# Kernel tuning notes

Hardware: AMD Instinct MI355X
Metric: run time of the kernel (lower is better)

The kernel has to match this reference:

```python
import jax, jax.numpy as jnp
import numpy as np

C = 256
C8 = C // 8

def setup_inputs() -> dict:
    key = jax.random.key(0)
    ks = jax.random.split(key, 8)
    B, H, W = 4, 64, 64
    x = jax.random.normal(ks[0], (B, C, H, W), dtype=jnp.float32)
    wq = jax.random.normal(ks[1], (C8, C), dtype=jnp.float32) * (1.0 / np.sqrt(C))
    bq = jnp.zeros((C8,), dtype=jnp.float32)
    wk = jax.random.normal(ks[2], (C8, C), dtype=jnp.float32) * (1.0 / np.sqrt(C))
    bk = jnp.zeros((C8,), dtype=jnp.float32)
    wv = jax.random.normal(ks[3], (C, C), dtype=jnp.float32) * (1.0 / np.sqrt(C))
    bv = jnp.zeros((C,), dtype=jnp.float32)
    gamma = jnp.ones((1,), dtype=jnp.float32) * 0.5  # nonzero so attention path contributes
    return {"x": x, "wq": wq, "bq": bq, "wk": wk, "bk": bk, "wv": wv, "bv": bv, "gamma": gamma}

def reference(x, wq, bq, wk, bk, wv, bv, gamma):
    B, Cc, Hh, Ww = x.shape
    N = Hh * Ww
    xf = x.reshape(B, Cc, N)  # [B,C,N]
    # 1x1 convs == per-pixel linear maps
    q = jnp.einsum('oc,bcn->bon', wq, xf) + bq[None, :, None]  # [B,C8,N]
    k = jnp.einsum('oc,bcn->bon', wk, xf) + bk[None, :, None]  # [B,C8,N]
    v = jnp.einsum('oc,bcn->bon', wv, xf) + bv[None, :, None]  # [B,C,N]
    # energy[b,n,m] = sum_c q[b,c,n] * k[b,c,m]  (unscaled)
    energy = jnp.einsum('bcn,bcm->bnm', q, k)
    attn = jax.nn.softmax(energy, axis=-1)
    # out[b,c,n] = sum_m v[b,c,m] * attn[b,n,m]
    out = jnp.einsum('bcm,bnm->bcn', v, attn).reshape(B, Cc, Hh, Ww)
    return gamma * out + x
```

## Files before the change

### kernel.cpp

```cpp
#include <hip/hip_runtime.h>
#include <hip/hip_fp16.h>

#define CC   256
#define QKC  32
#define NPIX 4096
#define NB   4
#define XSTR 264
#define VSTR 72

typedef __attribute__((ext_vector_type(8))) _Float16 f16x8;
typedef __attribute__((ext_vector_type(4))) float     f32x4;

__global__ __launch_bounds__(256) void wh_prep(
    const float* __restrict__ wq, const float* __restrict__ wk,
    const float* __restrict__ wv, __half* __restrict__ Wh)
{
    const int idx4 = blockIdx.x * 256 + threadIdx.x;
    const int o  = idx4 >> 6;
    const int cw = (idx4 & 63) << 2;
    const float* src;
    if (o < 256)      src = wv + (size_t)o * 256 + cw;
    else if (o < 288) src = wq + (size_t)(o - 256) * 256 + cw;
    else              src = wk + (size_t)(o - 288) * 256 + cw;
    const float4 v = *reinterpret_cast<const float4*>(src);
    __half h[4] = {__float2half(v.x), __float2half(v.y),
                   __float2half(v.z), __float2half(v.w)};
    *reinterpret_cast<uint2*>(Wh + (size_t)o * 256 + cw) =
        *reinterpret_cast<const uint2*>(h);
}

__global__ __launch_bounds__(512) void qkv_mfma(
    const float* __restrict__ x, const __half* __restrict__ Wh,
    const float* __restrict__ bq, const float* __restrict__ bk,
    const float* __restrict__ bv,
    __half* __restrict__ Qh, __half* __restrict__ Kh, __half* __restrict__ VTh)
{
    __shared__ __align__(16) __half sm[CC * VSTR];
    __half* xT   = sm;
    __half* vres = sm;

    const int t  = threadIdx.x;
    const int b  = blockIdx.x >> 6;
    const int n0 = (blockIdx.x & 63) << 6;

    {
        const int nl4 = t & 15;
        const int c0  = t >> 4;
        const float* xp = x + ((size_t)b * CC) * NPIX + n0 + nl4 * 4;
        #pragma unroll
        for (int i = 0; i < 8; ++i) {
            const int c = c0 + 32 * i;
            const float4 v = *reinterpret_cast<const float4*>(xp + (size_t)c * NPIX);
            xT[(nl4 * 4 + 0) * XSTR + c] = __float2half(v.x);
            xT[(nl4 * 4 + 1) * XSTR + c] = __float2half(v.y);
            xT[(nl4 * 4 + 2) * XSTR + c] = __float2half(v.z);
            xT[(nl4 * 4 + 3) * XSTR + c] = __float2half(v.w);
        }
    }
    __syncthreads();

    const int w = t >> 6, l = t & 63, lr = l & 15, s = l >> 4;
    const int nto = (w < 4) ? 3 : 2;
    const int ob0 = 32 * w, ob1 = 32 * w + 16, ob2 = 256 + 16 * w;

    f16x8 wf[3][8];
    #pragma unroll
    for (int kk = 0; kk < 8; ++kk) {
        wf[0][kk] = *reinterpret_cast<const f16x8*>(
            Wh + (size_t)(ob0 + lr) * 256 + kk * 32 + s * 8);
        wf[1][kk] = *reinterpret_cast<const f16x8*>(
            Wh + (size_t)(ob1 + lr) * 256 + kk * 32 + s * 8);
    }
    if (w < 4)
        #pragma unroll
        for (int kk = 0; kk < 8; ++kk)
            wf[2][kk] = *reinterpret_cast<const f16x8*>(
                Wh + (size_t)(ob2 + lr) * 256 + kk * 32 + s * 8);

    f32x4 acc[3][4];
    #pragma unroll
    for (int j = 0; j < 3; ++j)
        #pragma unroll
        for (int nt = 0; nt < 4; ++nt) acc[j][nt] = (f32x4){0.f, 0.f, 0.f, 0.f};

    #pragma unroll
    for (int nt = 0; nt < 4; ++nt) {
        f16x8 xf[8];
        #pragma unroll
        for (int kk = 0; kk < 8; ++kk)
            xf[kk] = *reinterpret_cast<const f16x8*>(
                &xT[(nt * 16 + lr) * XSTR + kk * 32 + s * 8]);
        #pragma unroll
        for (int j = 0; j < 3; ++j)
            if (j < nto)
                #pragma unroll
                for (int kk = 0; kk < 8; ++kk)
                    acc[j][nt] = __builtin_amdgcn_mfma_f32_16x16x32_f16(
                        xf[kk], wf[j][kk], acc[j][nt], 0, 0, 0);
    }

    if (w < 4) {
        const bool is_q = (w < 2);
        const int oc = (w & 1) * 16 + lr;
        __half* dst = is_q ? Qh : Kh;
        const float bias = (is_q ? bq : bk)[oc];
        #pragma unroll
        for (int nt = 0; nt < 4; ++nt)
            #pragma unroll
            for (int r = 0; r < 4; ++r) {
                const size_t n = (size_t)b * NPIX + n0 + nt * 16 + s * 4 + r;
                dst[n * QKC + oc] = __float2half(acc[2][nt][r] + bias);
            }
    }

    __syncthreads();
    {
        #pragma unroll
        for (int j = 0; j < 2; ++j) {
            const int c = 32 * w + 16 * j + lr;
            const float bias = bv[c];
            #pragma unroll
            for (int nt = 0; nt < 4; ++nt) {
                __half h[4];
                #pragma unroll
                for (int r = 0; r < 4; ++r) h[r] = __float2half(acc[j][nt][r] + bias);
                *reinterpret_cast<uint2*>(&vres[c * VSTR + nt * 16 + s * 4]) =
                    *reinterpret_cast<const uint2*>(h);
            }
        }
    }
    __syncthreads();
    {
        const int c = t >> 1, half = t & 1;
        __half* dst = VTh + ((size_t)(b * CC + c)) * NPIX + n0 + half * 32;
        #pragma unroll
        for (int jj = 0; jj < 4; ++jj)
            *reinterpret_cast<uint4*>(dst + jj * 8) =
                *reinterpret_cast<const uint4*>(&vres[c * VSTR + half * 32 + jj * 8]);
    }
}

__global__ __launch_bounds__(512) void attn_mfma(
    const __half* __restrict__ Qh, const __half* __restrict__ Kh,
    const __half* __restrict__ VTh, const float* __restrict__ x,
    const float* __restrict__ gamma, float* __restrict__ out)
{
    __shared__ unsigned char Praw[2][64 * 128];
    __shared__ float abuf[2][64];
    __shared__ float lbuf[64];

    const int t  = threadIdx.x;
    const int w  = t >> 6;
    const int l  = t & 63;
    const int lr = l & 15;
    const int s  = l >> 4;

    const int blk = (blockIdx.x & 7) * 32 + (blockIdx.x >> 3);
    const int b  = blk >> 6;
    const int n0 = (blk & 63) << 6;

    const int qw = w * 16 + lr;
    f16x8 qfrag;
    f16x8 kf[4];
    float m_run = -1e30f, l_run = 0.f;
    const __half* kbase = Kh + ((size_t)b * NPIX + lr) * QKC + s * 8;

    const int cbase = 64 * (w - 4);
    const __half* vbase = VTh + ((size_t)(b * CC + cbase + lr)) * NPIX + s * 8;
    f16x8 vfc[4][2], vfn[4][2];
    f32x4 O[4][4];
    #pragma unroll
    for (int ct = 0; ct < 4; ++ct)
        #pragma unroll
        for (int qt = 0; qt < 4; ++qt)
            O[ct][qt] = (f32x4){0.f, 0.f, 0.f, 0.f};

    auto do_softmax = [&](int bw) {
        f32x4 sacc[4];
        #pragma unroll
        for (int mt = 0; mt < 4; ++mt)
            sacc[mt] = __builtin_amdgcn_mfma_f32_16x16x32_f16(
                kf[mt], qfrag, (f32x4){0.f, 0.f, 0.f, 0.f}, 0, 0, 0);
        float tmax = sacc[0][0];
        #pragma unroll
        for (int mt = 0; mt < 4; ++mt)
            #pragma unroll
            for (int r = 0; r < 4; ++r) tmax = fmaxf(tmax, sacc[mt][r]);
        tmax = fmaxf(tmax, __shfl_xor(tmax, 16));
        tmax = fmaxf(tmax, __shfl_xor(tmax, 32));
        const float mnew = fmaxf(m_run, tmax);
        const float al   = __expf(m_run - mnew);
        float p[4][4];
        float lsum = 0.f;
        #pragma unroll
        for (int mt = 0; mt < 4; ++mt)
            #pragma unroll
            for (int r = 0; r < 4; ++r) {
                p[mt][r] = __expf(sacc[mt][r] - mnew);
                lsum += p[mt][r];
            }
        lsum += __shfl_xor(lsum, 16);
        lsum += __shfl_xor(lsum, 32);
        l_run = al * l_run + lsum;
        m_run = mnew;
        unsigned char* pb = &Praw[bw][0];
        #pragma unroll
        for (int mt = 0; mt < 4; ++mt) {
            const int g = ((s >> 1) + 2 * mt) ^ (qw & 7);
            const __half2 u0 = __floats2half2_rn(p[mt][0], p[mt][1]);
            const __half2 u1 = __floats2half2_rn(p[mt][2], p[mt][3]);
            *reinterpret_cast<__half2*>(pb + qw * 128 + g * 16 + (s & 1) * 8)     = u0;
            *reinterpret_cast<__half2*>(pb + qw * 128 + g * 16 + (s & 1) * 8 + 4) = u1;
        }
        if (l < 16) abuf[bw][qw] = al;
    };

    if (w < 4) {
        qfrag = *reinterpret_cast<const f16x8*>(
            Qh + ((size_t)b * NPIX + n0 + qw) * QKC + s * 8);
        #pragma unroll
        for (int mt = 0; mt < 4; ++mt)
            kf[mt] = *reinterpret_cast<const f16x8*>(kbase + (size_t)(mt * 16) * QKC);
        do_softmax(0);
        #pragma unroll
        for (int mt = 0; mt < 4; ++mt)
            kf[mt] = *reinterpret_cast<const f16x8*>(kbase + (size_t)(64 + mt * 16) * QKC);
    } else {
        #pragma unroll
        for (int ct = 0; ct < 4; ++ct)
            #pragma unroll
            for (int ks = 0; ks < 2; ++ks)
                vfc[ct][ks] = *reinterpret_cast<const f16x8*>(
                    vbase + (size_t)ct * 16 * NPIX + ks * 32);
    }
    __syncthreads();

    for (int step = 0; step < 64; ++step) {
        const int pbuf = step & 1;
        if (w < 4) {
            if (step < 63) {
                do_softmax(pbuf ^ 1);
                if (step < 62) {
                    const size_t moff = (size_t)((step + 2) * 64) * QKC;
                    #pragma unroll
                    for (int mt = 0; mt < 4; ++mt)
                        kf[mt] = *reinterpret_cast<const f16x8*>(
                            kbase + moff + (size_t)(mt * 16) * QKC);
                }
            }
        } else {
            if (step < 63) {
                const size_t moff = (size_t)((step + 1) * 64);
                #pragma unroll
                for (int ct = 0; ct < 4; ++ct)
                    #pragma unroll
                    for (int ks = 0; ks < 2; ++ks)
                        vfn[ct][ks] = *reinterpret_cast<const f16x8*>(
                            vbase + (size_t)ct * 16 * NPIX + moff + ks * 32);
            }
            float av[4];
            #pragma unroll
            for (int qt = 0; qt < 4; ++qt) av[qt] = abuf[pbuf][qt * 16 + lr];
            #pragma unroll
            for (int ct = 0; ct < 4; ++ct)
                #pragma unroll
                for (int qt = 0; qt < 4; ++qt)
                    #pragma unroll
                    for (int r = 0; r < 4; ++r) O[ct][qt][r] *= av[qt];

            const unsigned char* pr = &Praw[pbuf][0];
            #pragma unroll
            for (int qt = 0; qt < 4; ++qt) {
                const int q2 = qt * 16 + lr;
                const int g0 = s ^ (q2 & 7);
                const int g1 = (s + 4) ^ (q2 & 7);
                const f16x8 pf0 = *reinterpret_cast<const f16x8*>(pr + q2 * 128 + g0 * 16);
                const f16x8 pf1 = *reinterpret_cast<const f16x8*>(pr + q2 * 128 + g1 * 16);
                #pragma unroll
                for (int ct = 0; ct < 4; ++ct) {
                    O[ct][qt] = __builtin_amdgcn_mfma_f32_16x16x32_f16(
                        vfc[ct][0], pf0, O[ct][qt], 0, 0, 0);
                    O[ct][qt] = __builtin_amdgcn_mfma_f32_16x16x32_f16(
                        vfc[ct][1], pf1, O[ct][qt], 0, 0, 0);
                }
            }
            if (step < 63) {
                #pragma unroll
                for (int ct = 0; ct < 4; ++ct)
                    #pragma unroll
                    for (int ks = 0; ks < 2; ++ks) vfc[ct][ks] = vfn[ct][ks];
            }
        }
        __syncthreads();
    }

    if (w < 4) { if (l < 16) lbuf[qw] = l_run; }
    __syncthreads();
    if (w >= 4) {
        const float g = gamma[0];
        float linv[4];
        #pragma unroll
        for (int qt = 0; qt < 4; ++qt) linv[qt] = g / lbuf[qt * 16 + lr];
        #pragma unroll
        for (int ct = 0; ct < 4; ++ct)
            #pragma unroll
            for (int qt = 0; qt < 4; ++qt)
                #pragma unroll
                for (int r = 0; r < 4; ++r) {
                    const int c = cbase + ct * 16 + s * 4 + r;
                    const size_t idx = ((size_t)(b * CC + c)) * NPIX + n0 + qt * 16 + lr;
                    out[idx] = O[ct][qt][r] * linv[qt] + x[idx];
                }
    }
}

extern "C" void kernel_launch(void* const* d_in, const int* in_sizes, int n_in,
                              void* d_out, int out_size, void* d_ws, size_t ws_size,
                              hipStream_t stream) {
    const float* x     = (const float*)d_in[0];
    const float* wq    = (const float*)d_in[1];
    const float* bq    = (const float*)d_in[2];
    const float* wk    = (const float*)d_in[3];
    const float* bk    = (const float*)d_in[4];
    const float* wv    = (const float*)d_in[5];
    const float* bv    = (const float*)d_in[6];
    const float* gamma = (const float*)d_in[7];
    float* out = (float*)d_out;

    __half* Wh  = (__half*)d_ws;
    __half* Qh  = Wh + (size_t)320 * 256;
    __half* Kh  = Qh + (size_t)NB * NPIX * QKC;
    __half* VTh = Kh + (size_t)NB * NPIX * QKC;

    hipLaunchKernelGGL(wh_prep, dim3(80), dim3(256), 0, stream, wq, wk, wv, Wh);
    hipLaunchKernelGGL(qkv_mfma, dim3(NB * 64), dim3(512), 0, stream,
                       x, Wh, bq, bk, bv, Qh, Kh, VTh);
    hipLaunchKernelGGL(attn_mfma, dim3(256), dim3(512), 0, stream,
                       Qh, Kh, VTh, x, gamma, out);
}
```

Baseline: 101.0 us.

## Use exp2 softmax with lazy rescaling and ping-pong V registers

Folds log2(e) into the Q weights and bias so the softmax can use the native exp2 instruction. The online softmax now computes each lane's local max and exponentials before any cross-lane reduction, and skips rescaling the O accumulator unless the running max grows by more than a threshold, which a per-wave flag in shared memory signals. The step loop is unrolled by two with ping-pong V register buffers, which removes the register copy at each step, and MFMA priority is raised during the PV product. The trade-off is extra exp2 and shuffle work per tile and fp16 P values that can reach up to 2^8 before normalisation, which risks precision.

```diff
diff --git a/kernel.cpp b/kernel.cpp
--- a/kernel.cpp
+++ b/kernel.cpp
@@ -7,9 +7,16 @@
 #define NB   4
 #define XSTR 264
 #define VSTR 72
+#define LOG2E 1.44269504088896340736f
+#define TAU  8.0f
 
 typedef __attribute__((ext_vector_type(8))) _Float16 f16x8;
 typedef __attribute__((ext_vector_type(4))) float     f32x4;
+
+static __device__ __forceinline__ unsigned h2bits(__half2 h) {
+    union { __half2 h; unsigned u; } cv; cv.h = h; return cv.u;
+}
+#define E2(x) __builtin_amdgcn_exp2f(x)
 
 __global__ __launch_bounds__(256) void wh_prep(
     const float* __restrict__ wq, const float* __restrict__ wk,
@@ -19,12 +26,13 @@
     const int o  = idx4 >> 6;
     const int cw = (idx4 & 63) << 2;
     const float* src;
+    float scale = 1.0f;
     if (o < 256)      src = wv + (size_t)o * 256 + cw;
-    else if (o < 288) src = wq + (size_t)(o - 256) * 256 + cw;
+    else if (o < 288) { src = wq + (size_t)(o - 256) * 256 + cw; scale = LOG2E; }
     else              src = wk + (size_t)(o - 288) * 256 + cw;
     const float4 v = *reinterpret_cast<const float4*>(src);
-    __half h[4] = {__float2half(v.x), __float2half(v.y),
-                   __float2half(v.z), __float2half(v.w)};
+    __half h[4] = {__float2half(v.x * scale), __float2half(v.y * scale),
+                   __float2half(v.z * scale), __float2half(v.w * scale)};
     *reinterpret_cast<uint2*>(Wh + (size_t)o * 256 + cw) =
         *reinterpret_cast<const uint2*>(h);
 }
@@ -103,7 +111,7 @@
         const bool is_q = (w < 2);
         const int oc = (w & 1) * 16 + lr;
         __half* dst = is_q ? Qh : Kh;
-        const float bias = (is_q ? bq : bk)[oc];
+        const float bias = is_q ? bq[oc] * LOG2E : bk[oc];
         #pragma unroll
         for (int nt = 0; nt < 4; ++nt)
             #pragma unroll
@@ -147,6 +155,7 @@
 {
     __shared__ unsigned char Praw[2][64 * 128];
     __shared__ float abuf[2][64];
+    __shared__ __align__(16) int fbuf[2][4];
     __shared__ float lbuf[64];
 
     const int t  = threadIdx.x;
@@ -167,7 +176,7 @@
 
     const int cbase = 64 * (w - 4);
     const __half* vbase = VTh + ((size_t)(b * CC + cbase + lr)) * NPIX + s * 8;
-    f16x8 vfc[4][2], vfn[4][2];
+    f16x8 vA[4][2], vB[4][2];
     f32x4 O[4][4];
     #pragma unroll
     for (int ct = 0; ct < 4; ++ct)
@@ -181,38 +190,103 @@
         for (int mt = 0; mt < 4; ++mt)
             sacc[mt] = __builtin_amdgcn_mfma_f32_16x16x32_f16(
                 kf[mt], qfrag, (f32x4){0.f, 0.f, 0.f, 0.f}, 0, 0, 0);
-        float tmax = sacc[0][0];
+        float v[16];
         #pragma unroll
         for (int mt = 0; mt < 4; ++mt)
             #pragma unroll
-            for (int r = 0; r < 4; ++r) tmax = fmaxf(tmax, sacc[mt][r]);
-        tmax = fmaxf(tmax, __shfl_xor(tmax, 16));
-        tmax = fmaxf(tmax, __shfl_xor(tmax, 32));
-        const float mnew = fmaxf(m_run, tmax);
-        const float al   = __expf(m_run - mnew);
-        float p[4][4];
-        float lsum = 0.f;
-        #pragma unroll
-        for (int mt = 0; mt < 4; ++mt)
-            #pragma unroll
-            for (int r = 0; r < 4; ++r) {
-                p[mt][r] = __expf(sacc[mt][r] - mnew);
-                lsum += p[mt][r];
-            }
-        lsum += __shfl_xor(lsum, 16);
-        lsum += __shfl_xor(lsum, 32);
-        l_run = al * l_run + lsum;
-        m_run = mnew;
+            for (int r = 0; r < 4; ++r) v[mt * 4 + r] = sacc[mt][r];
+        float t8[8], t4[4], t2[2];
+        #pragma unroll
+        for (int i = 0; i < 8; ++i) t8[i] = fmaxf(v[i], v[i + 8]);
+        #pragma unroll
+        for (int i = 0; i < 4; ++i) t4[i] = fmaxf(t8[i], t8[i + 4]);
+        t2[0] = fmaxf(t4[0], t4[2]); t2[1] = fmaxf(t4[1], t4[3]);
+        const float m_l = fmaxf(t2[0], t2[1]);
+        float p[16];
+        #pragma unroll
+        for (int i = 0; i < 16; ++i) p[i] = E2(v[i] - m_l);
+        float s8[8], s4[4], s2[2];
+        #pragma unroll
+        for (int i = 0; i < 8; ++i) s8[i] = p[i] + p[i + 8];
+        #pragma unroll
+        for (int i = 0; i < 4; ++i) s4[i] = s8[i] + s8[i + 4];
+        s2[0] = s4[0] + s4[2]; s2[1] = s4[1] + s4[3];
+        const float e_l = s2[0] + s2[1];
+        float m_p = __shfl_xor(m_l, 16);
+        float e_p = __shfl_xor(e_l, 16);
+        const float m1 = fmaxf(m_l, m_p);
+        const float e1 = e_l * E2(m_l - m1) + e_p * E2(m_p - m1);
+        m_p = __shfl_xor(m1, 32);
+        e_p = __shfl_xor(e1, 32);
+        const float m_g = fmaxf(m1, m_p);
+        const float e_g = e1 * E2(m1 - m_g) + e_p * E2(m_p - m_g);
+        const bool need = (m_g - m_run) > TAU;
+        float f;
+        if (__any(need)) {
+            const float mnew = fmaxf(m_run, m_g);
+            const float al   = E2(m_run - mnew);
+            l_run = al * l_run + e_g * E2(m_g - mnew);
+            f = E2(m_l - mnew);
+            if (l < 16) abuf[bw][qw] = al;
+            if (l == 0) fbuf[bw][w] = 1;
+            m_run = mnew;
+        } else {
+            l_run += e_g * E2(m_g - m_run);
+            f = E2(m_l - m_run);
+            if (l < 16) abuf[bw][qw] = 1.0f;
+            if (l == 0) fbuf[bw][w] = 0;
+        }
         unsigned char* pb = &Praw[bw][0];
         #pragma unroll
         for (int mt = 0; mt < 4; ++mt) {
             const int g = ((s >> 1) + 2 * mt) ^ (qw & 7);
-            const __half2 u0 = __floats2half2_rn(p[mt][0], p[mt][1]);
-            const __half2 u1 = __floats2half2_rn(p[mt][2], p[mt][3]);
-            *reinterpret_cast<__half2*>(pb + qw * 128 + g * 16 + (s & 1) * 8)     = u0;
-            *reinterpret_cast<__half2*>(pb + qw * 128 + g * 16 + (s & 1) * 8 + 4) = u1;
-        }
-        if (l < 16) abuf[bw][qw] = al;
+            uint2 u;
+            u.x = h2bits(__floats2half2_rn(p[mt * 4 + 0] * f, p[mt * 4 + 1] * f));
+            u.y = h2bits(__floats2half2_rn(p[mt * 4 + 2] * f, p[mt * 4 + 3] * f));
+            *reinterpret_cast<uint2*>(pb + qw * 128 + g * 16 + (s & 1) * 8) = u;
+        }
+    };
+
+    auto vload = [&](f16x8 (&dst)[4][2], int m0) {
+        #pragma unroll
+        for (int ct = 0; ct < 4; ++ct)
+            #pragma unroll
+            for (int ks = 0; ks < 2; ++ks)
+                dst[ct][ks] = *reinterpret_cast<const f16x8*>(
+                    vbase + (size_t)ct * 16 * NPIX + m0 + ks * 32);
+    };
+
+    auto pv_body = [&](int pbuf, f16x8 (&vf)[4][2]) {
+        const int4 fl = *reinterpret_cast<const int4*>(&fbuf[pbuf][0]);
+        if (fl.x | fl.y | fl.z | fl.w) {
+            float av[4];
+            #pragma unroll
+            for (int qt = 0; qt < 4; ++qt) av[qt] = abuf[pbuf][qt * 16 + lr];
+            #pragma unroll
+            for (int ct = 0; ct < 4; ++ct)
+                #pragma unroll
+                for (int qt = 0; qt < 4; ++qt)
+                    #pragma unroll
+                    for (int r = 0; r < 4; ++r) O[ct][qt][r] *= av[qt];
+        }
+        const unsigned char* pr = &Praw[pbuf][0];
+        __builtin_amdgcn_s_setprio(1);
+        #pragma unroll
+        for (int qt = 0; qt < 4; ++qt) {
+            const int q2 = qt * 16 + lr;
+            const int g0 = s ^ (q2 & 7);
+            const int g1 = (s + 4) ^ (q2 & 7);
+            const f16x8 pf0 = *reinterpret_cast<const f16x8*>(pr + q2 * 128 + g0 * 16);
+            const f16x8 pf1 = *reinterpret_cast<const f16x8*>(pr + q2 * 128 + g1 * 16);
+            #pragma unroll
+            for (int ct = 0; ct < 4; ++ct) {
+                O[ct][qt] = __builtin_amdgcn_mfma_f32_16x16x32_f16(
+                    vf[ct][0], pf0, O[ct][qt], 0, 0, 0);
+                O[ct][qt] = __builtin_amdgcn_mfma_f32_16x16x32_f16(
+                    vf[ct][1], pf1, O[ct][qt], 0, 0, 0);
+            }
+        }
+        __builtin_amdgcn_s_setprio(0);
     };
 
     if (w < 4) {
@@ -226,22 +300,32 @@
         for (int mt = 0; mt < 4; ++mt)
             kf[mt] = *reinterpret_cast<const f16x8*>(kbase + (size_t)(64 + mt * 16) * QKC);
     } else {
-        #pragma unroll
-        for (int ct = 0; ct < 4; ++ct)
-            #pragma unroll
-            for (int ks = 0; ks < 2; ++ks)
-                vfc[ct][ks] = *reinterpret_cast<const f16x8*>(
-                    vbase + (size_t)ct * 16 * NPIX + ks * 32);
-    }
-    __syncthreads();
-
-    for (int step = 0; step < 64; ++step) {
-        const int pbuf = step & 1;
+        vload(vA, 0);
+    }
+    __syncthreads();
+
+    for (int it = 0; it < 32; ++it) {
+        const int se = 2 * it;
         if (w < 4) {
-            if (step < 63) {
-                do_softmax(pbuf ^ 1);
-                if (step < 62) {
-                    const size_t moff = (size_t)((step + 2) * 64) * QKC;
+            do_softmax(1);
+            if (se < 62) {
+                const size_t moff = (size_t)((se + 2) * 64) * QKC;
+                #pragma unroll
+                for (int mt = 0; mt < 4; ++mt)
+                    kf[mt] = *reinterpret_cast<const f16x8*>(
+                        kbase + moff + (size_t)(mt * 16) * QKC);
+            }
+        } else {
+            vload(vB, (se + 1) * 64);
+            pv_body(0, vA);
+        }
+        __syncthreads();
+        const int so = se + 1;
+        if (w < 4) {
+            if (so < 63) {
+                do_softmax(0);
+                if (so < 62) {
+                    const size_t moff = (size_t)((so + 2) * 64) * QKC;
                     #pragma unroll
                     for (int mt = 0; mt < 4; ++mt)
                         kf[mt] = *reinterpret_cast<const f16x8*>(
@@ -249,47 +333,8 @@
                 }
             }
         } else {
-            if (step < 63) {
-                const size_t moff = (size_t)((step + 1) * 64);
-                #pragma unroll
-                for (int ct = 0; ct < 4; ++ct)
-                    #pragma unroll
-                    for (int ks = 0; ks < 2; ++ks)
-                        vfn[ct][ks] = *reinterpret_cast<const f16x8*>(
-                            vbase + (size_t)ct * 16 * NPIX + moff + ks * 32);
-            }
-            float av[4];
-            #pragma unroll
-            for (int qt = 0; qt < 4; ++qt) av[qt] = abuf[pbuf][qt * 16 + lr];
-            #pragma unroll
-            for (int ct = 0; ct < 4; ++ct)
-                #pragma unroll
-                for (int qt = 0; qt < 4; ++qt)
-                    #pragma unroll
-                    for (int r = 0; r < 4; ++r) O[ct][qt][r] *= av[qt];
-
-            const unsigned char* pr = &Praw[pbuf][0];
-            #pragma unroll
-            for (int qt = 0; qt < 4; ++qt) {
-                const int q2 = qt * 16 + lr;
-                const int g0 = s ^ (q2 & 7);
-                const int g1 = (s + 4) ^ (q2 & 7);
-                const f16x8 pf0 = *reinterpret_cast<const f16x8*>(pr + q2 * 128 + g0 * 16);
-                const f16x8 pf1 = *reinterpret_cast<const f16x8*>(pr + q2 * 128 + g1 * 16);
-                #pragma unroll
-                for (int ct = 0; ct < 4; ++ct) {
-                    O[ct][qt] = __builtin_amdgcn_mfma_f32_16x16x32_f16(
-                        vfc[ct][0], pf0, O[ct][qt], 0, 0, 0);
-                    O[ct][qt] = __builtin_amdgcn_mfma_f32_16x16x32_f16(
-                        vfc[ct][1], pf1, O[ct][qt], 0, 0, 0);
-                }
-            }
-            if (step < 63) {
-                #pragma unroll
-                for (int ct = 0; ct < 4; ++ct)
-                    #pragma unroll
-                    for (int ks = 0; ks < 2; ++ks) vfc[ct][ks] = vfn[ct][ks];
-            }
+            if (so < 63) vload(vA, (so + 1) * 64);
+            pv_body(1, vB);
         }
         __syncthreads();
     }
```

Measured after the change: 108.2 us. 7.1% more time.
